# Optimization experiments

Measured on AMD Instinct MI355X. Metric: run time of the kernel, lower is better.

The kernel has to match this reference:

```python
import jax, jax.numpy as jnp
import numpy as np
import math

HEAD = 4
B, N, C = 8, 1024, 256


def setup_inputs() -> dict:
    key = jax.random.key(0)
    k1, k2, k3, k4, k5 = jax.random.split(key, 5)
    query = jax.random.normal(k1, (B, N, C), dtype=jnp.float32)
    keyt = jax.random.normal(k2, (B, N, C), dtype=jnp.float32)
    value = jax.random.normal(k3, (B, N, C), dtype=jnp.float32)
    mask = jax.random.randint(k4, (B, N, N), 0, 2).astype(bool)
    dis = jax.random.normal(k5, (B, N, N), dtype=jnp.float32)
    return {"query": query, "key": keyt, "value": value, "mask": mask, "dis": dis}


def reference(query, key, value, mask, dis):
    Bq, Nq, Cq = key.shape
    d = Cq // HEAD
    # split heads: [B,N,C] -> [h,B,N,d]
    q = query.reshape(Bq, Nq, HEAD, d).transpose(2, 0, 1, 3)
    k = key.reshape(Bq, Nq, HEAD, d).transpose(2, 0, 1, 3)
    v = value.reshape(Bq, Nq, HEAD, d).transpose(2, 0, 1, 3)
    # scores: [h,B,N,N]; note: dis added BEFORE scaling, as in the torch code
    scores = jnp.einsum('hbnd,hbmd->hbnm', q, k)
    scores = scores + dis[None]            # dis broadcasts over head dim
    scores = scores / math.sqrt(d)
    scores = jnp.where(mask[None], -jnp.inf, scores)
    p_attn = jax.nn.softmax(scores, axis=-1)
    out = jnp.einsum('hbnm,hbmd->hbnd', p_attn, v)  # [h,B,N,d]
    out = out.transpose(1, 2, 0, 3).reshape(Bq, Nq, Cq)
    return out, p_attn
```

## Files before the change

### kernel.cpp

```cpp
#include <hip/hip_runtime.h>
#include <math.h>

#define HEADS 4
#define BATCH 8
#define SEQ   1024
#define CH    256
#define DH    64
#define RB    16
#define NTHR  512
#define SSTR  1032

typedef float  floatx4  __attribute__((ext_vector_type(4)));
typedef short  shortx8  __attribute__((ext_vector_type(8)));

__device__ __forceinline__ unsigned short f2bf(float f) {
    unsigned u = __float_as_uint(f);
    unsigned r = u + 0x7FFFu + ((u >> 16) & 1u);
    return (unsigned short)(r >> 16);
}
__device__ __forceinline__ float bf2f(unsigned short h) {
    return __uint_as_float(((unsigned)h) << 16);
}
__device__ __forceinline__ shortx8 pack8(float4 a, float4 b) {
    shortx8 r;
    r[0] = (short)f2bf(a.x); r[1] = (short)f2bf(a.y);
    r[2] = (short)f2bf(a.z); r[3] = (short)f2bf(a.w);
    r[4] = (short)f2bf(b.x); r[5] = (short)f2bf(b.y);
    r[6] = (short)f2bf(b.z); r[7] = (short)f2bf(b.w);
    return r;
}

__global__ __launch_bounds__(256)
void prep(const float* __restrict__ q, const float* __restrict__ k,
          const float* __restrict__ v, unsigned short* __restrict__ qb,
          unsigned short* __restrict__ kb, unsigned short* __restrict__ vt)
{
    const int t = threadIdx.x;
    const int bid = blockIdx.x;
    if (bid < 2048) {
        const float* src = (bid < 1024) ? q : k;
        unsigned short* dst = (bid < 1024) ? qb : kb;
        size_t idx = (size_t)(bid & 1023) * 2048 + (size_t)t * 8;
        float4 a = *(const float4*)(src + idx);
        float4 b = *(const float4*)(src + idx + 4);
        *(shortx8*)(dst + idx) = pack8(a, b);
        return;
    }
    __shared__ unsigned short tl[64][68];
    const int vb = bid - 2048;
    const int nt = vb & 15, h = (vb >> 4) & 3, b = vb >> 6;
    const int n0 = nt * 64;
    const float* vsrc = v + ((size_t)(b * SEQ + n0)) * CH + h * DH;
    #pragma unroll
    for (int it = 0; it < 4; ++it) {
        int fid = it * 256 + t;
        int n = fid >> 4, cc = (fid & 15) * 4;
        float4 x = *(const float4*)(vsrc + (size_t)n * CH + cc);
        tl[n][cc]     = f2bf(x.x);
        tl[n][cc + 1] = f2bf(x.y);
        tl[n][cc + 2] = f2bf(x.z);
        tl[n][cc + 3] = f2bf(x.w);
    }
    __syncthreads();
    unsigned short* vout = vt + ((size_t)((b * HEADS + h) * DH)) * SEQ + n0;
    #pragma unroll
    for (int it = 0; it < 2; ++it) {
        int cid = it * 256 + t;
        int d = cid >> 3, nc = cid & 7;
        shortx8 r;
        #pragma unroll
        for (int j = 0; j < 8; ++j) r[j] = (short)tl[nc * 8 + j][d];
        *(shortx8*)(vout + (size_t)d * SEQ + nc * 8) = r;
    }
}

__global__ __launch_bounds__(NTHR, 8)
void attn_mfma(const unsigned short* __restrict__ qb,
               const unsigned short* __restrict__ kbf,
               const unsigned short* __restrict__ vt,
               const void* __restrict__ maskp,
               const float* __restrict__ dis, float* __restrict__ out,
               float* __restrict__ pout)
{
    __shared__ unsigned short Sraw[RB][SSTR];
    __shared__ float Opart[RB][65];
    __shared__ float invs[RB];

    const int t   = threadIdx.x;
    const int bid = blockIdx.x;
    const int nb  = bid & 63;
    const int hb  = bid >> 6;
    const int b   = hb & (BATCH - 1);
    const int h   = hb >> 3;
    const int n0  = nb * RB;

    const int lane = t & 63;
    const int w    = t >> 6;
    const int ln   = lane & 15;
    const int qd   = lane >> 4;

    int fl;
    {
        const unsigned* mw = (const unsigned*)maskp;
        int found = 0;
        #pragma unroll
        for (int j = 0; j < 16; ++j)
            if (mw[lane * 16 + j] & 0xFFFFFF00u) found = 1;
        fl = (__ballot(found != 0) != 0ULL) ? 1 : 0;
    }
    const unsigned char* mask8  = (const unsigned char*)maskp;
    const int*           mask32 = (const int*)maskp;

    const unsigned short* qrow = qb + ((size_t)(b * SEQ + n0 + ln)) * CH + h * DH;
    shortx8 aq0 = *(const shortx8*)(qrow + qd * 8);
    shortx8 aq1 = *(const shortx8*)(qrow + 32 + qd * 8);

    const unsigned short* kbase = kbf + ((size_t)(b * SEQ)) * CH + h * DH;
    const unsigned short* vbase = vt + ((size_t)((b * HEADS + h) * DH)) * SEQ;

    #pragma unroll 2
    for (int mc = 0; mc < 8; ++mc) {
        const int mg = mc * 128 + w * 16 + ln;
        const size_t dibase = ((size_t)(b * SEQ + n0 + qd * 4)) * SEQ + mg;
        float dv[4]; int mk[4];
        #pragma unroll
        for (int r = 0; r < 4; ++r) dv[r] = dis[dibase + (size_t)r * SEQ];
        if (fl) {
            #pragma unroll
            for (int r = 0; r < 4; ++r) mk[r] = mask8[dibase + (size_t)r * SEQ];
        } else {
            #pragma unroll
            for (int r = 0; r < 4; ++r) mk[r] = mask32[dibase + (size_t)r * SEQ];
        }
        const unsigned short* krow = kbase + (size_t)mg * CH;
        shortx8 b0 = *(const shortx8*)(krow + qd * 8);
        shortx8 b1 = *(const shortx8*)(krow + 32 + qd * 8);
        floatx4 acc = {0.f, 0.f, 0.f, 0.f};
        acc = __builtin_amdgcn_mfma_f32_16x16x32_bf16(aq0, b0, acc, 0, 0, 0);
        acc = __builtin_amdgcn_mfma_f32_16x16x32_bf16(aq1, b1, acc, 0, 0, 0);
        #pragma unroll
        for (int r = 0; r < 4; ++r) {
            float sc = mk[r] ? -INFINITY : (acc[r] + dv[r]) * 0.125f;
            Sraw[qd * 4 + r][mg] = f2bf(sc);
        }
    }
    __syncthreads();

    {
        const int r = t >> 5, l = t & 31;
        float mx = -INFINITY;
        #pragma unroll
        for (int j = 0; j < 4; ++j) {
            shortx8 sv = *(const shortx8*)&Sraw[r][j * 256 + l * 8];
            #pragma unroll
            for (int e = 0; e < 8; ++e) mx = fmaxf(mx, bf2f((unsigned short)sv[e]));
        }
        #pragma unroll
        for (int off = 16; off; off >>= 1) mx = fmaxf(mx, __shfl_xor(mx, off, 32));
        float sum = 0.f;
        #pragma unroll
        for (int j = 0; j < 4; ++j) {
            shortx8 sv = *(const shortx8*)&Sraw[r][j * 256 + l * 8];
            shortx8 ev;
            #pragma unroll
            for (int e = 0; e < 8; ++e) {
                float x = __expf(bf2f((unsigned short)sv[e]) - mx);
                sum += x;
                ev[e] = (short)f2bf(x);
            }
            *(shortx8*)&Sraw[r][j * 256 + l * 8] = ev;
        }
        #pragma unroll
        for (int off = 16; off; off >>= 1) sum += __shfl_xor(sum, off, 32);
        if (l == 0) invs[r] = 1.0f / sum;
    }
    __syncthreads();

    {
        float* prow = pout + ((size_t)((h * BATCH + b) * SEQ + n0)) * SEQ;
        #pragma unroll
        for (int i = 0; i < RB; ++i) {
            const float inv = invs[i];
            unsigned pk = *(const unsigned*)&Sraw[i][t * 2];
            float2 pv = { bf2f((unsigned short)(pk & 0xFFFFu)) * inv,
                          bf2f((unsigned short)(pk >> 16)) * inv };
            *(float2*)(prow + (size_t)i * SEQ + t * 2) = pv;
        }
    }

    const int hm = w >> 2;
    const int c  = (w & 3) * 16;
    floatx4 acco = {0.f, 0.f, 0.f, 0.f};
    const unsigned short* vcol = vbase + (size_t)(c + ln) * SEQ;
    #pragma unroll 2
    for (int mc = 0; mc < 8; ++mc) {
        #pragma unroll
        for (int s = 0; s < 2; ++s) {
            const int kk = hm * 512 + mc * 64 + s * 32 + qd * 8;
            shortx8 af  = *(const shortx8*)&Sraw[ln][kk];
            shortx8 bfv = *(const shortx8*)(vcol + kk);
            acco = __builtin_amdgcn_mfma_f32_16x16x32_bf16(af, bfv, acco, 0, 0, 0);
        }
    }
    if (hm == 1) {
        #pragma unroll
        for (int r = 0; r < 4; ++r) Opart[qd * 4 + r][c + ln] = acco[r];
    }
    __syncthreads();
    if (hm == 0) {
        #pragma unroll
        for (int r = 0; r < 4; ++r) {
            int row = qd * 4 + r;
            out[((size_t)(b * SEQ + n0 + row)) * CH + h * DH + c + ln]
                = (acco[r] + Opart[row][c + ln]) * invs[row];
        }
    }
}

extern "C" void kernel_launch(void* const* d_in, const int* in_sizes, int n_in,
                              void* d_out, int out_size, void* d_ws, size_t ws_size,
                              hipStream_t stream) {
    const float* q    = (const float*)d_in[0];
    const float* k    = (const float*)d_in[1];
    const float* v    = (const float*)d_in[2];
    const void*  mask = d_in[3];
    const float* dis  = (const float*)d_in[4];
    float* out  = (float*)d_out;
    float* pout = out + (size_t)BATCH * SEQ * CH;

    unsigned short* qb  = (unsigned short*)d_ws;
    unsigned short* kbw = qb  + (size_t)BATCH * SEQ * CH;
    unsigned short* vtw = kbw + (size_t)BATCH * SEQ * CH;
    (void)ws_size;

    prep<<<2560, 256, 0, stream>>>(q, k, v, qb, kbw, vtw);
    attn_mfma<<<HEADS * BATCH * (SEQ / RB), NTHR, 0, stream>>>(
        qb, kbw, vtw, mask, dis, out, pout);
}
```

Before: 275.5 us.

## Loop over heads per block to reuse dis and mask loads across heads

Each block now handles all four heads for its 16-row tile. It loads the dis values and mask bits into registers once and reuses them for every head, instead of re-reading them from global memory per head. This removes the repeated dis and mask traffic, which scales with the head count. Probability and output writes now use nontemporal stores. The trade-off is a grid four times smaller (512 blocks), higher register use (the launch bound hint drops from 8 to 4) and serialised head work inside each block, all of which reduce latency hiding.

```diff
diff --git a/kernel.cpp b/kernel.cpp
--- a/kernel.cpp
+++ b/kernel.cpp
@@ -11,6 +11,7 @@
 #define SSTR  1032
 
 typedef float  floatx4  __attribute__((ext_vector_type(4)));
+typedef float  floatx2  __attribute__((ext_vector_type(2)));
 typedef short  shortx8  __attribute__((ext_vector_type(8)));
 
 __device__ __forceinline__ unsigned short f2bf(float f) {
@@ -74,7 +75,7 @@
     }
 }
 
-__global__ __launch_bounds__(NTHR, 8)
+__global__ __launch_bounds__(NTHR, 4)
 void attn_mfma(const unsigned short* __restrict__ qb,
                const unsigned short* __restrict__ kbf,
                const unsigned short* __restrict__ vt,
@@ -88,10 +89,8 @@
 
     const int t   = threadIdx.x;
     const int bid = blockIdx.x;
-    const int nb  = bid & 63;
-    const int hb  = bid >> 6;
-    const int b   = hb & (BATCH - 1);
-    const int h   = hb >> 3;
+    const int b   = bid & (BATCH - 1);
+    const int nb  = bid >> 3;
     const int n0  = nb * RB;
 
     const int lane = t & 63;
@@ -111,108 +110,125 @@
     const unsigned char* mask8  = (const unsigned char*)maskp;
     const int*           mask32 = (const int*)maskp;
 
-    const unsigned short* qrow = qb + ((size_t)(b * SEQ + n0 + ln)) * CH + h * DH;
-    shortx8 aq0 = *(const shortx8*)(qrow + qd * 8);
-    shortx8 aq1 = *(const shortx8*)(qrow + 32 + qd * 8);
-
-    const unsigned short* kbase = kbf + ((size_t)(b * SEQ)) * CH + h * DH;
-    const unsigned short* vbase = vt + ((size_t)((b * HEADS + h) * DH)) * SEQ;
-
-    #pragma unroll 2
-    for (int mc = 0; mc < 8; ++mc) {
-        const int mg = mc * 128 + w * 16 + ln;
-        const size_t dibase = ((size_t)(b * SEQ + n0 + qd * 4)) * SEQ + mg;
-        float dv[4]; int mk[4];
-        #pragma unroll
-        for (int r = 0; r < 4; ++r) dv[r] = dis[dibase + (size_t)r * SEQ];
-        if (fl) {
-            #pragma unroll
-            for (int r = 0; r < 4; ++r) mk[r] = mask8[dibase + (size_t)r * SEQ];
-        } else {
-            #pragma unroll
-            for (int r = 0; r < 4; ++r) mk[r] = mask32[dibase + (size_t)r * SEQ];
-        }
-        const unsigned short* krow = kbase + (size_t)mg * CH;
-        shortx8 b0 = *(const shortx8*)(krow + qd * 8);
-        shortx8 b1 = *(const shortx8*)(krow + 32 + qd * 8);
-        floatx4 acc = {0.f, 0.f, 0.f, 0.f};
-        acc = __builtin_amdgcn_mfma_f32_16x16x32_bf16(aq0, b0, acc, 0, 0, 0);
-        acc = __builtin_amdgcn_mfma_f32_16x16x32_bf16(aq1, b1, acc, 0, 0, 0);
-        #pragma unroll
-        for (int r = 0; r < 4; ++r) {
-            float sc = mk[r] ? -INFINITY : (acc[r] + dv[r]) * 0.125f;
-            Sraw[qd * 4 + r][mg] = f2bf(sc);
-        }
-    }
-    __syncthreads();
-
+    float dreg[32];
+    unsigned mbits = 0;
     {
-        const int r = t >> 5, l = t & 31;
-        float mx = -INFINITY;
-        #pragma unroll
-        for (int j = 0; j < 4; ++j) {
-            shortx8 sv = *(const shortx8*)&Sraw[r][j * 256 + l * 8];
-            #pragma unroll
-            for (int e = 0; e < 8; ++e) mx = fmaxf(mx, bf2f((unsigned short)sv[e]));
-        }
-        #pragma unroll
-        for (int off = 16; off; off >>= 1) mx = fmaxf(mx, __shfl_xor(mx, off, 32));
-        float sum = 0.f;
-        #pragma unroll
-        for (int j = 0; j < 4; ++j) {
-            shortx8 sv = *(const shortx8*)&Sraw[r][j * 256 + l * 8];
-            shortx8 ev;
-            #pragma unroll
-            for (int e = 0; e < 8; ++e) {
-                float x = __expf(bf2f((unsigned short)sv[e]) - mx);
-                sum += x;
-                ev[e] = (short)f2bf(x);
-            }
-            *(shortx8*)&Sraw[r][j * 256 + l * 8] = ev;
-        }
-        #pragma unroll
-        for (int off = 16; off; off >>= 1) sum += __shfl_xor(sum, off, 32);
-        if (l == 0) invs[r] = 1.0f / sum;
-    }
-    __syncthreads();
-
-    {
-        float* prow = pout + ((size_t)((h * BATCH + b) * SEQ + n0)) * SEQ;
-        #pragma unroll
-        for (int i = 0; i < RB; ++i) {
-            const float inv = invs[i];
-            unsigned pk = *(const unsigned*)&Sraw[i][t * 2];
-            float2 pv = { bf2f((unsigned short)(pk & 0xFFFFu)) * inv,
-                          bf2f((unsigned short)(pk >> 16)) * inv };
-            *(float2*)(prow + (size_t)i * SEQ + t * 2) = pv;
-        }
-    }
-
-    const int hm = w >> 2;
-    const int c  = (w & 3) * 16;
-    floatx4 acco = {0.f, 0.f, 0.f, 0.f};
-    const unsigned short* vcol = vbase + (size_t)(c + ln) * SEQ;
-    #pragma unroll 2
-    for (int mc = 0; mc < 8; ++mc) {
-        #pragma unroll
-        for (int s = 0; s < 2; ++s) {
-            const int kk = hm * 512 + mc * 64 + s * 32 + qd * 8;
-            shortx8 af  = *(const shortx8*)&Sraw[ln][kk];
-            shortx8 bfv = *(const shortx8*)(vcol + kk);
-            acco = __builtin_amdgcn_mfma_f32_16x16x32_bf16(af, bfv, acco, 0, 0, 0);
-        }
-    }
-    if (hm == 1) {
-        #pragma unroll
-        for (int r = 0; r < 4; ++r) Opart[qd * 4 + r][c + ln] = acco[r];
-    }
-    __syncthreads();
-    if (hm == 0) {
-        #pragma unroll
-        for (int r = 0; r < 4; ++r) {
-            int row = qd * 4 + r;
-            out[((size_t)(b * SEQ + n0 + row)) * CH + h * DH + c + ln]
-                = (acco[r] + Opart[row][c + ln]) * invs[row];
+        const size_t dib0 = ((size_t)(b * SEQ + n0 + qd * 4)) * SEQ + w * 16 + ln;
+        #pragma unroll
+        for (int mc = 0; mc < 8; ++mc) {
+            #pragma unroll
+            for (int r = 0; r < 4; ++r) {
+                const size_t idx = dib0 + (size_t)r * SEQ + mc * 128;
+                dreg[mc * 4 + r] = dis[idx];
+                int mk = fl ? (int)mask8[idx] : mask32[idx];
+                mbits |= (mk ? 1u : 0u) << (mc * 4 + r);
+            }
+        }
+    }
+
+    #pragma unroll 1
+    for (int h = 0; h < HEADS; ++h) {
+        const unsigned short* qrow =
+            qb + ((size_t)(b * SEQ + n0 + ln)) * CH + h * DH;
+        shortx8 aq0 = *(const shortx8*)(qrow + qd * 8);
+        shortx8 aq1 = *(const shortx8*)(qrow + 32 + qd * 8);
+
+        const unsigned short* kbase = kbf + ((size_t)(b * SEQ)) * CH + h * DH;
+        const unsigned short* vbase = vt + ((size_t)((b * HEADS + h) * DH)) * SEQ;
+
+        #pragma unroll
+        for (int mc = 0; mc < 8; ++mc) {
+            const int mg = mc * 128 + w * 16 + ln;
+            const unsigned short* krow = kbase + (size_t)mg * CH;
+            shortx8 b0 = *(const shortx8*)(krow + qd * 8);
+            shortx8 b1 = *(const shortx8*)(krow + 32 + qd * 8);
+            floatx4 acc = {0.f, 0.f, 0.f, 0.f};
+            acc = __builtin_amdgcn_mfma_f32_16x16x32_bf16(aq0, b0, acc, 0, 0, 0);
+            acc = __builtin_amdgcn_mfma_f32_16x16x32_bf16(aq1, b1, acc, 0, 0, 0);
+            #pragma unroll
+            for (int r = 0; r < 4; ++r) {
+                float sc = ((mbits >> (mc * 4 + r)) & 1u)
+                               ? -INFINITY
+                               : (acc[r] + dreg[mc * 4 + r]) * 0.125f;
+                Sraw[qd * 4 + r][mg] = f2bf(sc);
+            }
+        }
+        __syncthreads();
+
+        {
+            const int r = t >> 5, l = t & 31;
+            float mx = -INFINITY;
+            #pragma unroll
+            for (int j = 0; j < 4; ++j) {
+                shortx8 sv = *(const shortx8*)&Sraw[r][j * 256 + l * 8];
+                #pragma unroll
+                for (int e = 0; e < 8; ++e)
+                    mx = fmaxf(mx, bf2f((unsigned short)sv[e]));
+            }
+            #pragma unroll
+            for (int off = 16; off; off >>= 1)
+                mx = fmaxf(mx, __shfl_xor(mx, off, 32));
+            float sum = 0.f;
+            #pragma unroll
+            for (int j = 0; j < 4; ++j) {
+                shortx8 sv = *(const shortx8*)&Sraw[r][j * 256 + l * 8];
+                shortx8 ev;
+                #pragma unroll
+                for (int e = 0; e < 8; ++e) {
+                    float x = __expf(bf2f((unsigned short)sv[e]) - mx);
+                    sum += x;
+                    ev[e] = (short)f2bf(x);
+                }
+                *(shortx8*)&Sraw[r][j * 256 + l * 8] = ev;
+            }
+            #pragma unroll
+            for (int off = 16; off; off >>= 1) sum += __shfl_xor(sum, off, 32);
+            if (l == 0) invs[r] = 1.0f / sum;
+        }
+        __syncthreads();
+
+        {
+            float* prow = pout + ((size_t)((h * BATCH + b) * SEQ + n0)) * SEQ;
+            #pragma unroll
+            for (int i = 0; i < RB; ++i) {
+                const float inv = invs[i];
+                unsigned pk = *(const unsigned*)&Sraw[i][t * 2];
+                floatx2 pv = { bf2f((unsigned short)(pk & 0xFFFFu)) * inv,
+                               bf2f((unsigned short)(pk >> 16)) * inv };
+                __builtin_nontemporal_store(
+                    pv, (floatx2*)(prow + (size_t)i * SEQ + t * 2));
+            }
+        }
+
+        const int hm = w >> 2;
+        const int c  = (w & 3) * 16;
+        floatx4 acco = {0.f, 0.f, 0.f, 0.f};
+        const unsigned short* vcol = vbase + (size_t)(c + ln) * SEQ;
+        #pragma unroll 2
+        for (int mc = 0; mc < 8; ++mc) {
+            #pragma unroll
+            for (int s = 0; s < 2; ++s) {
+                const int kk = hm * 512 + mc * 64 + s * 32 + qd * 8;
+                shortx8 af  = *(const shortx8*)&Sraw[ln][kk];
+                shortx8 bfv = *(const shortx8*)(vcol + kk);
+                acco = __builtin_amdgcn_mfma_f32_16x16x32_bf16(af, bfv, acco,
+                                                               0, 0, 0);
+            }
+        }
+        if (hm == 1) {
+            #pragma unroll
+            for (int r = 0; r < 4; ++r) Opart[qd * 4 + r][c + ln] = acco[r];
+        }
+        __syncthreads();
+        if (hm == 0) {
+            #pragma unroll
+            for (int r = 0; r < 4; ++r) {
+                int row = qd * 4 + r;
+                float ov = (acco[r] + Opart[row][c + ln]) * invs[row];
+                __builtin_nontemporal_store(
+                    ov, out + ((size_t)(b * SEQ + n0 + row)) * CH
+                            + h * DH + c + ln);
+            }
         }
     }
 }
@@ -234,6 +250,6 @@
     (void)ws_size;
 
     prep<<<2560, 256, 0, stream>>>(q, k, v, qb, kbw, vtw);
-    attn_mfma<<<HEADS * BATCH * (SEQ / RB), NTHR, 0, stream>>>(
+    attn_mfma<<<BATCH * (SEQ / RB), NTHR, 0, stream>>>(
         qb, kbw, vtw, mask, dis, out, pout);
 }
```

After: 269.2 us. 1.02x faster.
